# Kernel optimization log

Measured on AMD Instinct MI355X. Metric: run time of the kernel, lower is better.

The kernel has to match this reference:

```python
import jax, jax.numpy as jnp
import numpy as np

IN_C, OUT_C, K, STRIDE, PAD, N_EXPERTS = 64, 128, 3, 1, 1, 4
B, H, W = 32, 64, 64


def setup_inputs() -> dict:
    key = jax.random.key(0)
    k1, k2, k3, k4 = jax.random.split(key, 4)
    x = jax.random.normal(k1, (B, IN_C, H, W), dtype=jnp.float32)
    idx = jax.random.randint(k2, (B,), 0, N_EXPERTS, dtype=jnp.int64)
    # Expert conv weights/biases (PyTorch Conv2d layout: [out_c, in_c, kh, kw])
    fan_in = IN_C * K * K
    bound = 1.0 / np.sqrt(fan_in)
    Wc = jax.random.uniform(k3, (N_EXPERTS, OUT_C, IN_C, K, K), dtype=jnp.float32,
                            minval=-bound, maxval=bound)
    bc = jax.random.uniform(k4, (N_EXPERTS, OUT_C), dtype=jnp.float32,
                            minval=-bound, maxval=bound)
    return {"x": x, "idx": idx, "Wc": Wc, "bc": bc}


def _conv2d(x, w, b):
    # x: [B, C_in, H, W], w: [C_out, C_in, K, K], b: [C_out]
    y = jax.lax.conv_general_dilated(
        x, w,
        window_strides=(STRIDE, STRIDE),
        padding=[(PAD, PAD), (PAD, PAD)],
        dimension_numbers=("NCHW", "OIHW", "NCHW"),
    )
    return y + b[None, :, None, None]


def reference(x, idx, Wc, bc):
    # Compute every expert's conv for every sample (faithful to the torch code),
    # then gather each sample's selected expert output.
    results = jax.vmap(lambda w, b: _conv2d(x, w, b))(Wc, bc)  # [E, B, C_out, H, W]
    results = jnp.moveaxis(results, 0, 1)                      # [B, E, C_out, H, W]
    out = jnp.take_along_axis(
        results, idx[:, None, None, None, None].astype(jnp.int32), axis=1
    )  # [B, 1, C_out, H, W]
    return jnp.squeeze(out, axis=1)
```

## Files before the change

### kernel.cpp

```cpp
#include <hip/hip_runtime.h>
#include <hip/hip_bf16.h>


#define IC 64
#define OC 128
#define HH 64
#define WW 64

typedef short short8 __attribute__((ext_vector_type(8)));
typedef ushort ushort8 __attribute__((ext_vector_type(8)));
typedef float float16 __attribute__((ext_vector_type(16)));

typedef const __attribute__((address_space(1))) void gas_t;
typedef __attribute__((address_space(3))) void las_t;

static __device__ __forceinline__ ushort f2bf(float v) {
    __hip_bfloat16 h = __float2bfloat16(v);
    return *(ushort*)&h;
}

__global__ __launch_bounds__(256)
void reorder_w(const float* __restrict__ Wc, ushort* __restrict__ wout) {
    __shared__ ushort lw[4 * 584];
    const int t   = threadIdx.x;
    const int e   = blockIdx.x >> 5;
    const int oc0 = (blockIdx.x & 31) * 4;
    const float* src = Wc + (size_t)(e * 128 + oc0) * 576;
#pragma unroll
    for (int k = 0; k < 9; ++k) {
        const int f   = k * 256 + t;
        const int ocl = f / 576;
        const int rem = f - ocl * 576;
        lw[ocl * 584 + rem] = f2bf(src[f]);
    }
    __syncthreads();
#pragma unroll
    for (int k = 0; k < 2; ++k) {
        const int n = k * 256 + t;
        if (n < 288) {
            const int ocl = n & 3, ich = (n >> 2) & 7, tap = n >> 5;
            ushort8 v;
#pragma unroll
            for (int icl = 0; icl < 8; ++icl)
                v[icl] = lw[ocl * 584 + (ich * 8 + icl) * 9 + tap];
            *(ushort8*)(wout +
                ((((size_t)(e * 9 + tap) * 8 + ich) * 128 + oc0 + ocl) * 8)) = v;
        }
    }
}

__global__ __launch_bounds__(512, 4)
void moe_conv_mfma(const float* __restrict__ x, const int* __restrict__ idx,
                   const ushort* __restrict__ wre, const float* __restrict__ bc,
                   float* __restrict__ out) {
    __shared__ __align__(16) ushort xs[6 * 8 * 66 * 8];
    __shared__ __align__(16) ushort wbuf[8192];
    __shared__ float bias[128];

    const int t = threadIdx.x;

    const int lin = blockIdx.x;
    const int nw  = (lin & 7) * 64 + (lin >> 3);
    const int b   = nw >> 4;
    const int rq  = nw & 15;
    const int row0 = rq * 4;
    const int e    = ((unsigned)idx[b]) & 3;

    const int lane31 = t & 31;
    const int lhi    = (t >> 5) & 1;
    const int wv     = t >> 6;
    const int w0     = wv & 1;
    const int pr     = wv >> 1;

    const ushort* we = wre + (size_t)e * 9 * 8192;

#pragma unroll
    for (int i = 0; i < 2; ++i) {
        __builtin_amdgcn_global_load_lds(
            (gas_t*)(we + i * 4096 + t * 8),
            (las_t*)&wbuf[i * 4096 + t * 8], 16, 0, 0);
    }

    if (t < 192) {
        const int r = t >> 5, rem = t & 31;
        const int ich = rem >> 2, side = (rem >> 1) & 1, q = rem & 1;
        const int hc = side ? 65 : 0;
        ushort4 z = {0, 0, 0, 0};
        *(ushort4*)&xs[(((r * 8 + ich) * 66 + hc) * 8 + q * 4)] = z;
    } else if (t < 320) {
        bias[t - 192] = bc[e * OC + (t - 192)];
    }

    const float* xb = x + (size_t)b * IC * HH * WW;
    {
        const int gc   = t & 63;
        const int csel = t >> 6;
#pragma unroll
        for (int it = 0; it < 12; ++it) {
            const int combo = it * 8 + csel;
            const int r = combo >> 4, rem = combo & 15;
            const int ich = rem >> 1, q = rem & 1;
            const int gr = row0 - 1 + r;
            ushort4 u = {0, 0, 0, 0};
            if ((unsigned)gr < (unsigned)HH) {
                const int ic0 = ich * 8 + q * 4;
                u.x = f2bf(xb[((ic0 + 0) * HH + gr) * WW + gc]);
                u.y = f2bf(xb[((ic0 + 1) * HH + gr) * WW + gc]);
                u.z = f2bf(xb[((ic0 + 2) * HH + gr) * WW + gc]);
                u.w = f2bf(xb[((ic0 + 3) * HH + gr) * WW + gc]);
            }
            *(ushort4*)&xs[(((r * 8 + ich) * 66 + (gc + 1)) * 8 + q * 4)] = u;
        }
    }

    float16 acc[2][2];
#pragma unroll
    for (int a = 0; a < 2; ++a)
#pragma unroll
        for (int cg = 0; cg < 2; ++cg)
#pragma unroll
            for (int r = 0; r < 16; ++r) acc[a][cg][r] = 0.0f;

#pragma unroll
    for (int tap = 0; tap < 9; ++tap) {
        asm volatile("s_waitcnt vmcnt(0) lgkmcnt(0)" ::: "memory");
        __builtin_amdgcn_s_barrier();

        const int kh = tap / 3;
        const int kw = tap - kh * 3;
        const int rr = pr + kh;
        const int hb = lane31 + kw;

        __builtin_amdgcn_s_setprio(1);
#pragma unroll
        for (int ks = 0; ks < 4; ++ks) {
            const int ich = ks * 2 + lhi;
            const short8 a0 = *(const short8*)&wbuf[(ich * 128 + w0 * 64 + lane31) * 8];
            const short8 a1 = *(const short8*)&wbuf[(ich * 128 + w0 * 64 + 32 + lane31) * 8];
            const short8 b0 = *(const short8*)&xs[((rr * 8 + ich) * 66 + hb) * 8];
            const short8 b1 = *(const short8*)&xs[((rr * 8 + ich) * 66 + hb + 32) * 8];
            acc[0][0] = __builtin_amdgcn_mfma_f32_32x32x16_bf16(a0, b0, acc[0][0], 0, 0, 0);
            acc[0][1] = __builtin_amdgcn_mfma_f32_32x32x16_bf16(a0, b1, acc[0][1], 0, 0, 0);
            acc[1][0] = __builtin_amdgcn_mfma_f32_32x32x16_bf16(a1, b0, acc[1][0], 0, 0, 0);
            acc[1][1] = __builtin_amdgcn_mfma_f32_32x32x16_bf16(a1, b1, acc[1][1], 0, 0, 0);
        }
        __builtin_amdgcn_s_setprio(0);

        __builtin_amdgcn_s_barrier();
        if (tap < 8) {
            const ushort* wt = we + (tap + 1) * 8192;
#pragma unroll
            for (int i = 0; i < 2; ++i) {
                __builtin_amdgcn_global_load_lds(
                    (gas_t*)(wt + i * 4096 + t * 8),
                    (las_t*)&wbuf[i * 4096 + t * 8], 16, 0, 0);
            }
        }
    }

#pragma unroll
    for (int a = 0; a < 2; ++a) {
        const int ocb = w0 * 64 + a * 32 + 4 * lhi;
#pragma unroll
        for (int reg = 0; reg < 16; ++reg) {
            const int oc = ocb + (reg & 3) + 8 * (reg >> 2);
            const float bv = bias[oc];
            const size_t base = (((size_t)b * OC + oc) * HH + (row0 + pr)) * WW;
            out[base + lane31]      = acc[a][0][reg] + bv;
            out[base + 32 + lane31] = acc[a][1][reg] + bv;
        }
    }
}

extern "C" void kernel_launch(void* const* d_in, const int* in_sizes, int n_in,
                              void* d_out, int out_size, void* d_ws, size_t ws_size,
                              hipStream_t stream) {
    const float* x   = (const float*)d_in[0];
    const int*   idx = (const int*)d_in[1];
    const float* Wc  = (const float*)d_in[2];
    const float* bc  = (const float*)d_in[3];
    float* out  = (float*)d_out;
    ushort* wre = (ushort*)d_ws;

    reorder_w<<<128, 256, 0, stream>>>(Wc, wre);
    moe_conv_mfma<<<512, 512, 0, stream>>>(x, idx, wre, bc, out);
}
```

Baseline: 112.0 us.

## Split weight tap buffer into two halves for finer-grained load/compute overlap

The weight staging buffer is split into two 4096-element halves, and the tap loop becomes 18 half-steps, each covering four input-channel groups. Each half-step waits with vmcnt(1) for only the older load, then refills the half it just consumed while the other half is in use. This replaces the old full drain before every tap, so global-to-LDS weight loads can overlap the MFMA work. The cost is twice as many barriers and smaller compute chunks between them.

New measurement: 112.1 us. Within noise of the previous version (+0.1%).

```diff
diff --git a/kernel.cpp b/kernel.cpp
--- a/kernel.cpp
+++ b/kernel.cpp
@@ -54,7 +54,7 @@
                    const ushort* __restrict__ wre, const float* __restrict__ bc,
                    float* __restrict__ out) {
     __shared__ __align__(16) ushort xs[6 * 8 * 66 * 8];
-    __shared__ __align__(16) ushort wbuf[8192];
+    __shared__ __align__(16) ushort wbuf[2][4096];
     __shared__ float bias[128];
 
     const int t = threadIdx.x;
@@ -74,12 +74,10 @@
 
     const ushort* we = wre + (size_t)e * 9 * 8192;
 
-#pragma unroll
-    for (int i = 0; i < 2; ++i) {
-        __builtin_amdgcn_global_load_lds(
-            (gas_t*)(we + i * 4096 + t * 8),
-            (las_t*)&wbuf[i * 4096 + t * 8], 16, 0, 0);
-    }
+    __builtin_amdgcn_global_load_lds((gas_t*)(we + t * 8),
+                                     (las_t*)&wbuf[0][t * 8], 16, 0, 0);
+    __builtin_amdgcn_global_load_lds((gas_t*)(we + 4096 + t * 8),
+                                     (las_t*)&wbuf[1][t * 8], 16, 0, 0);
 
     if (t < 192) {
         const int r = t >> 5, rem = t & 31;
@@ -122,21 +120,28 @@
             for (int r = 0; r < 16; ++r) acc[a][cg][r] = 0.0f;
 
 #pragma unroll
-    for (int tap = 0; tap < 9; ++tap) {
-        asm volatile("s_waitcnt vmcnt(0) lgkmcnt(0)" ::: "memory");
+    for (int j = 0; j < 18; ++j) {
+        if (j == 0)
+            asm volatile("s_waitcnt vmcnt(1) lgkmcnt(0)" ::: "memory");
+        else if (j < 17)
+            asm volatile("s_waitcnt vmcnt(1)" ::: "memory");
+        else
+            asm volatile("s_waitcnt vmcnt(0)" ::: "memory");
         __builtin_amdgcn_s_barrier();
 
-        const int kh = tap / 3;
-        const int kw = tap - kh * 3;
-        const int rr = pr + kh;
-        const int hb = lane31 + kw;
+        const int tap = j >> 1;
+        const int kh  = tap / 3;
+        const int kw  = tap - kh * 3;
+        const int rr  = pr + kh;
+        const int hb  = lane31 + kw;
 
         __builtin_amdgcn_s_setprio(1);
 #pragma unroll
-        for (int ks = 0; ks < 4; ++ks) {
-            const int ich = ks * 2 + lhi;
-            const short8 a0 = *(const short8*)&wbuf[(ich * 128 + w0 * 64 + lane31) * 8];
-            const short8 a1 = *(const short8*)&wbuf[(ich * 128 + w0 * 64 + 32 + lane31) * 8];
+        for (int kss = 0; kss < 2; ++kss) {
+            const int ich  = (j & 1) * 4 + kss * 2 + lhi;
+            const int ichl = kss * 2 + lhi;
+            const short8 a0 = *(const short8*)&wbuf[j & 1][(ichl * 128 + w0 * 64 + lane31) * 8];
+            const short8 a1 = *(const short8*)&wbuf[j & 1][(ichl * 128 + w0 * 64 + 32 + lane31) * 8];
             const short8 b0 = *(const short8*)&xs[((rr * 8 + ich) * 66 + hb) * 8];
             const short8 b1 = *(const short8*)&xs[((rr * 8 + ich) * 66 + hb + 32) * 8];
             acc[0][0] = __builtin_amdgcn_mfma_f32_32x32x16_bf16(a0, b0, acc[0][0], 0, 0, 0);
@@ -147,14 +152,10 @@
         __builtin_amdgcn_s_setprio(0);
 
         __builtin_amdgcn_s_barrier();
-        if (tap < 8) {
-            const ushort* wt = we + (tap + 1) * 8192;
-#pragma unroll
-            for (int i = 0; i < 2; ++i) {
-                __builtin_amdgcn_global_load_lds(
-                    (gas_t*)(wt + i * 4096 + t * 8),
-                    (las_t*)&wbuf[i * 4096 + t * 8], 16, 0, 0);
-            }
+        if (j < 16) {
+            __builtin_amdgcn_global_load_lds(
+                (gas_t*)(we + (j + 2) * 4096 + t * 8),
+                (las_t*)&wbuf[j & 1][t * 8], 16, 0, 0);
         }
     }
 
```
